# Performance work log

Hardware: AMD Instinct MI355X
Metric: run time of the kernel (lower is better)

Reference implementation:

```python
import jax, jax.numpy as jnp
import numpy as np

TEMPERATURE = 0.1

def setup_inputs() -> dict:
    key = jax.random.key(0)
    k1, k2 = jax.random.split(key)
    A = jax.random.normal(k1, (16, 2048, 256), dtype=jnp.float32)
    B = jax.random.normal(k2, (16, 2048, 256), dtype=jnp.float32)
    return {"A": A, "B": B}

def _l2norm(x):
    # F.normalize(p=2, dim=-1): x / max(||x||, eps), eps=1e-12
    n = jnp.sqrt(jnp.sum(x * x, axis=-1, keepdims=True))
    return x / jnp.maximum(n, 1e-12)

def _nce_dir(sim):
    # sim: (B, N, N) logits; labels are the diagonal (row n -> col n)
    # mean over all B*N rows of (logsumexp(row) - row[label])
    lse = jax.nn.logsumexp(sim, axis=-1)            # (B, N)
    diag = jnp.diagonal(sim, axis1=-2, axis2=-1)    # (B, N)
    return jnp.mean(lse - diag)

def reference(A, B):
    emb1 = _l2norm(A)
    emb2 = _l2norm(B)
    sim12 = jnp.einsum("bnc,bmc->bnm", emb1, emb2) / TEMPERATURE  # (B, N, N)
    # sim21 is sim12 transposed per batch; reuse instead of a second bmm
    sim21 = jnp.swapaxes(sim12, -1, -2)
    return _nce_dir(sim12) + _nce_dir(sim21)
```

## Files before the change

### kernel.cpp

```cpp
#include <hip/hip_runtime.h>
#include <hip/hip_bf16.h>

typedef __attribute__((ext_vector_type(8))) __bf16 bf16x8;
typedef __attribute__((ext_vector_type(16))) float f32x16;

#define SCALE_L2E 14.4269504088896f
#define NTOT 32768

#define AS_GLOBAL __attribute__((address_space(1)))
#define AS_LDS    __attribute__((address_space(3)))

__device__ inline void async_copy16(const void* g, void* l) {
    __builtin_amdgcn_global_load_lds((const AS_GLOBAL void*)g, (AS_LDS void*)l, 16, 0, 0);
}

__device__ inline unsigned int f2bf(float f) {
    unsigned int u = __builtin_bit_cast(unsigned int, f);
    u += 0x7fffu + ((u >> 16) & 1u);
    return u >> 16;
}

__device__ inline uint4 pack8(float4 x, float4 y, float s) {
    uint4 r;
    r.x = f2bf(x.x * s) | (f2bf(x.y * s) << 16);
    r.y = f2bf(x.z * s) | (f2bf(x.w * s) << 16);
    r.z = f2bf(y.x * s) | (f2bf(y.y * s) << 16);
    r.w = f2bf(y.z * s) | (f2bf(y.w * s) << 16);
    return r;
}

__device__ inline float dot8(float4 x, float4 y) {
    return x.x*y.x + x.y*y.y + x.z*y.z + x.w*y.w;
}

__global__ __launch_bounds__(256) void nrm_kernel(
        const float* __restrict__ A, const float* __restrict__ B,
        uint4* __restrict__ E1f, uint4* __restrict__ E2f,
        float* __restrict__ diagPart, float* __restrict__ scalars,
        unsigned int* __restrict__ counter) {
    const int tid = threadIdx.x, w = tid >> 6, l = tid & 63;
    const int q = l & 31, h = l >> 5;
    const int wid = blockIdx.x * 4 + w;

    const float4* A4 = (const float4*)A + ((size_t)wid * 8 + h) * 64 + q * 2;
    const float4* B4 = (const float4*)B + ((size_t)wid * 8 + h) * 64 + q * 2;

    float4 a[8], bb[8];
    #pragma unroll
    for (int i = 0; i < 4; ++i) {
        a[2*i]    = A4[i * 128];
        a[2*i+1]  = A4[i * 128 + 1];
        bb[2*i]   = B4[i * 128];
        bb[2*i+1] = B4[i * 128 + 1];
    }

    float ddAcc = 0.f;
    #pragma unroll
    for (int i = 0; i < 4; ++i) {
        float sa = dot8(a[2*i], a[2*i]) + dot8(a[2*i+1], a[2*i+1]);
        float sb = dot8(bb[2*i], bb[2*i]) + dot8(bb[2*i+1], bb[2*i+1]);
        float dd = dot8(a[2*i], bb[2*i]) + dot8(a[2*i+1], bb[2*i+1]);
        #pragma unroll
        for (int off = 1; off <= 16; off <<= 1) {
            sa += __shfl_xor(sa, off);
            sb += __shfl_xor(sb, off);
            dd += __shfl_xor(dd, off);
        }
        const float ia = 1.0f / fmaxf(sqrtf(sa), 1e-12f);
        const float ib = 1.0f / fmaxf(sqrtf(sb), 1e-12f);
        if (q == 0) ddAcc += dd * ia * ib * 10.0f;

        const int n0 = wid * 8 + i * 2 + h;
        const size_t chunk = (size_t)(n0 >> 11) * 65536
                           + (size_t)((n0 & 2047) >> 5) * 1024
                           + (q >> 1) * 64 + (q & 1) * 32 + (n0 & 31);
        E1f[chunk] = pack8(a[2*i], a[2*i+1], ia * SCALE_L2E);
        E2f[chunk] = pack8(bb[2*i], bb[2*i+1], ib);
    }

    #pragma unroll
    for (int off = 1; off <= 32; off <<= 1) ddAcc += __shfl_xor(ddAcc, off);
    __shared__ float part[4];
    if (l == 0) part[w] = ddAcc;
    __syncthreads();
    if (tid == 0) diagPart[blockIdx.x] = part[0] + part[1] + part[2] + part[3];
    if (blockIdx.x == 0 && tid == 0) { scalars[0] = 0.f; *counter = 0u; }
}

__global__ __launch_bounds__(256, 2) void gemm_kernel(
        const bf16x8* __restrict__ E1f, const uint4* __restrict__ E2f,
        float* __restrict__ colPart, float* __restrict__ rowPart) {
    __shared__ bf16x8 Bbuf[2][2048];
    __shared__ float colLDS[2048];

    const int tid = threadIdx.x, w = tid >> 6, l = tid & 63;
    const int b = blockIdx.x & 15;
    const int ct = (blockIdx.x >> 4) & 3, rt = blockIdx.x >> 6;

    for (int i = l; i < 512; i += 64) colLDS[w * 512 + i] = 0.f;

    const uint4* Bb = E2f + (size_t)b * 65536 + (size_t)ct * 16384 + l;

    auto stage = [&](int buf, int sg) {
        const uint4* src = Bb + (size_t)sg * 2048 + (w * 8) * 64;
        #pragma unroll
        for (int j = 0; j < 8; ++j)
            async_copy16(src + j * 64, &Bbuf[buf][(w * 8 + j) * 64]);
    };

    stage(0, 0);

    const bf16x8* Af0 = E1f + (size_t)b * 65536 + (size_t)(rt * 8 + w * 2) * 1024 + l;
    const bf16x8* Af1 = Af0 + 1024;
    bf16x8 af0[16], af1[16];
    #pragma unroll
    for (int kt = 0; kt < 16; ++kt) { af0[kt] = Af0[kt * 64]; af1[kt] = Af1[kt * 64]; }

    float rowAcc0[16], rowAcc1[16];
    #pragma unroll
    for (int r = 0; r < 16; ++r) { rowAcc0[r] = 0.f; rowAcc1[r] = 0.f; }

    __syncthreads();

    for (int sg = 0; sg < 8; ++sg) {
        if (sg < 7) stage((sg + 1) & 1, sg + 1);

        const bf16x8* Bf = Bbuf[sg & 1];
        for (int half = 0; half < 2; ++half) {
            f32x16 acc0, acc1;
            #pragma unroll
            for (int r = 0; r < 16; ++r) { acc0[r] = 0.f; acc1[r] = 0.f; }

            #pragma unroll
            for (int kt = 0; kt < 16; ++kt) {
                bf16x8 bfrag = Bf[half * 1024 + kt * 64 + l];
                acc0 = __builtin_amdgcn_mfma_f32_32x32x16_bf16(af0[kt], bfrag, acc0, 0, 0, 0);
                acc1 = __builtin_amdgcn_mfma_f32_32x32x16_bf16(af1[kt], bfrag, acc1, 0, 0, 0);
            }

            float p = 0.f;
            #pragma unroll
            for (int r = 0; r < 16; ++r) {
                float e0 = exp2f(acc0[r] - SCALE_L2E);
                float e1 = exp2f(acc1[r] - SCALE_L2E);
                rowAcc0[r] += e0;
                rowAcc1[r] += e1;
                p += e0 + e1;
            }
            p += __shfl_xor(p, 32);
            if (l < 32) colLDS[w * 512 + (sg * 2 + half) * 32 + l] += p;
        }
        __syncthreads();
    }

    #pragma unroll
    for (int r = 0; r < 16; ++r) {
        #pragma unroll
        for (int off = 1; off <= 16; off <<= 1) {
            rowAcc0[r] += __shfl_xor(rowAcc0[r], off);
            rowAcc1[r] += __shfl_xor(rowAcc1[r], off);
        }
    }
    if ((l & 31) == 0) {
        float* rs = rowPart + (size_t)(b * 4 + ct) * 2048 + rt * 256 + w * 64 + 4 * (l >> 5);
        #pragma unroll
        for (int r = 0; r < 16; ++r) {
            const int rl = (r & 3) + 8 * (r >> 2);
            rs[rl]      = rowAcc0[r];
            rs[rl + 32] = rowAcc1[r];
        }
    }

    __syncthreads();
    float* gcol = colPart + (size_t)((b * 4 + ct) * 8 + rt) * 512;
    for (int i = tid; i < 512; i += 256)
        gcol[i] = colLDS[i] + colLDS[512 + i] + colLDS[1024 + i] + colLDS[1536 + i];
}

__global__ __launch_bounds__(256) void fin_kernel(
        const float* __restrict__ colPart, const float* __restrict__ rowPart,
        const float* __restrict__ diagPart, float* __restrict__ scalars,
        unsigned int* __restrict__ counter, float* __restrict__ out) {
    const int tid = threadIdx.x;
    float s = 0.f;
    #pragma unroll
    for (int k = 0; k < 2; ++k) {
        const int g = blockIdx.x * 512 + k * 256 + tid;
        const float* cp = colPart + (size_t)(((g >> 11) * 4 + ((g >> 9) & 3)) * 8) * 512 + (g & 511);
        float cs = 0.f;
        #pragma unroll
        for (int rt = 0; rt < 8; ++rt) cs += cp[rt * 512];
        const float* rp = rowPart + (size_t)(g >> 11) * 4 * 2048 + (g & 2047);
        float rsum = rp[0] + rp[2048] + rp[4096] + rp[6144];
        s += logf(cs) + logf(rsum);
    }
    #pragma unroll
    for (int off = 1; off <= 32; off <<= 1) s += __shfl_xor(s, off);
    __shared__ float part[4];
    __shared__ unsigned int lastFlag;
    if ((tid & 63) == 0) part[tid >> 6] = s;
    __syncthreads();
    if (tid == 0) {
        atomicAdd(&scalars[0], part[0] + part[1] + part[2] + part[3]);
        __threadfence();
        lastFlag = (atomicAdd(counter, 1u) == 63u) ? 1u : 0u;
    }
    __syncthreads();
    if (lastFlag) {
        float d = diagPart[tid] + diagPart[tid + 256]
                + diagPart[tid + 512] + diagPart[tid + 768];
        #pragma unroll
        for (int off = 1; off <= 32; off <<= 1) d += __shfl_xor(d, off);
        if ((tid & 63) == 0) part[tid >> 6] = d;
        __syncthreads();
        if (tid == 0) {
            const float diag = part[0] + part[1] + part[2] + part[3];
            const float logSum = atomicAdd(&scalars[0], 0.f);
            out[0] = (logSum - 2.0f * diag) / (float)NTOT + 20.0f;
        }
    }
}

extern "C" void kernel_launch(void* const* d_in, const int* in_sizes, int n_in,
                              void* d_out, int out_size, void* d_ws, size_t ws_size,
                              hipStream_t stream) {
    const float* A = (const float*)d_in[0];
    const float* B = (const float*)d_in[1];

    char* w = (char*)d_ws;
    uint4* E1f = (uint4*)w;
    uint4* E2f = (uint4*)(w + (size_t)16 * 1024 * 1024);
    float* colPart = (float*)(w + (size_t)32 * 1024 * 1024);
    float* rowPart = colPart + 262144;
    float* diagPart = rowPart + 131072;
    float* scalars = diagPart + 1024;
    unsigned int* counter = (unsigned int*)(scalars + 1);

    hipLaunchKernelGGL(nrm_kernel, dim3(1024), dim3(256), 0, stream,
                       A, B, E1f, E2f, diagPart, scalars, counter);
    hipLaunchKernelGGL(gemm_kernel, dim3(512), dim3(256), 0, stream,
                       (const bf16x8*)E1f, (const uint4*)E2f, colPart, rowPart);
    hipLaunchKernelGGL(fin_kernel, dim3(64), dim3(256), 0, stream,
                       colPart, rowPart, diagPart, scalars, counter, (float*)d_out);
}
```

Baseline: 157.6 us.

## Software-pipeline MFMA tiles with exp epilogue using double accumulators

The per-stage loop now computes the MFMA tile for one half while the exp/row/column-sum epilogue of the previous half runs. Two sets of accumulators make this possible, and it is meant to overlap matrix-core work with transcendental VALU work. MFMA sections are wrapped in s_setprio to favour matrix issue. The epilogue uses the raw hardware exp2 intrinsic without the constant max-shift subtraction, and the final +20 correction is dropped to match. The extra accumulators raise VGPR/AGPR pressure, which could cause spills or lower occupancy.

Measured after the change: 159.0 us. Within noise of the previous version (+0.9%).

```diff
diff --git a/kernel.cpp b/kernel.cpp
--- a/kernel.cpp
+++ b/kernel.cpp
@@ -120,38 +120,48 @@
     #pragma unroll
     for (int r = 0; r < 16; ++r) { rowAcc0[r] = 0.f; rowAcc1[r] = 0.f; }
 
+    f32x16 aA0, aA1, aB0, aB1;
+
+    auto mm = [&](f32x16& c0, f32x16& c1, int sg, int half) {
+        const bf16x8* Bf = Bbuf[sg & 1] + half * 1024 + l;
+        #pragma unroll
+        for (int r = 0; r < 16; ++r) { c0[r] = 0.f; c1[r] = 0.f; }
+        __builtin_amdgcn_s_setprio(1);
+        #pragma unroll
+        for (int kt = 0; kt < 16; ++kt) {
+            bf16x8 bfrag = Bf[kt * 64];
+            c0 = __builtin_amdgcn_mfma_f32_32x32x16_bf16(af0[kt], bfrag, c0, 0, 0, 0);
+            c1 = __builtin_amdgcn_mfma_f32_32x32x16_bf16(af1[kt], bfrag, c1, 0, 0, 0);
+        }
+        __builtin_amdgcn_s_setprio(0);
+    };
+
+    auto epi = [&](const f32x16& c0, const f32x16& c1, int slot) {
+        float p0 = 0.f, p1 = 0.f;
+        #pragma unroll
+        for (int r = 0; r < 16; ++r) {
+            float e0 = __builtin_amdgcn_exp2f(c0[r]);
+            float e1 = __builtin_amdgcn_exp2f(c1[r]);
+            rowAcc0[r] += e0;
+            rowAcc1[r] += e1;
+            p0 += e0; p1 += e1;
+        }
+        float p = p0 + p1;
+        p += __shfl_xor(p, 32);
+        if (l < 32) colLDS[w * 512 + slot * 32 + l] += p;
+    };
+
     __syncthreads();
 
     for (int sg = 0; sg < 8; ++sg) {
         if (sg < 7) stage((sg + 1) & 1, sg + 1);
-
-        const bf16x8* Bf = Bbuf[sg & 1];
-        for (int half = 0; half < 2; ++half) {
-            f32x16 acc0, acc1;
-            #pragma unroll
-            for (int r = 0; r < 16; ++r) { acc0[r] = 0.f; acc1[r] = 0.f; }
-
-            #pragma unroll
-            for (int kt = 0; kt < 16; ++kt) {
-                bf16x8 bfrag = Bf[half * 1024 + kt * 64 + l];
-                acc0 = __builtin_amdgcn_mfma_f32_32x32x16_bf16(af0[kt], bfrag, acc0, 0, 0, 0);
-                acc1 = __builtin_amdgcn_mfma_f32_32x32x16_bf16(af1[kt], bfrag, acc1, 0, 0, 0);
-            }
-
-            float p = 0.f;
-            #pragma unroll
-            for (int r = 0; r < 16; ++r) {
-                float e0 = exp2f(acc0[r] - SCALE_L2E);
-                float e1 = exp2f(acc1[r] - SCALE_L2E);
-                rowAcc0[r] += e0;
-                rowAcc1[r] += e1;
-                p += e0 + e1;
-            }
-            p += __shfl_xor(p, 32);
-            if (l < 32) colLDS[w * 512 + (sg * 2 + half) * 32 + l] += p;
-        }
+        mm(aA0, aA1, sg, 0);
+        if (sg) epi(aB0, aB1, sg * 2 - 1);
+        mm(aB0, aB1, sg, 1);
+        epi(aA0, aA1, sg * 2);
         __syncthreads();
     }
+    epi(aB0, aB1, 15);
 
     #pragma unroll
     for (int r = 0; r < 16; ++r) {
@@ -216,7 +226,7 @@
         if (tid == 0) {
             const float diag = part[0] + part[1] + part[2] + part[3];
             const float logSum = atomicAdd(&scalars[0], 0.f);
-            out[0] = (logSum - 2.0f * diag) / (float)NTOT + 20.0f;
+            out[0] = (logSum - 2.0f * diag) / (float)NTOT;
         }
     }
 }
```
